# Performance work log

Hardware: AMD Instinct MI355X
Metric: run time of the kernel (lower is better)

## Reference

```python
import jax, jax.numpy as jnp
import numpy as np

BETA = 0.25
DECAY = 0.99
EPS = 1e-05
N_E = 1024
E_DIM = 64

def setup_inputs() -> dict:
    key = jax.random.key(0)
    k1, k2, k3, k4 = jax.random.split(key, 4)
    z = jax.random.normal(k1, (32, 64, 32, 32), dtype=jnp.float32)
    embedding = jax.random.normal(k2, (N_E, E_DIM), dtype=jnp.float32)
    cluster_size = jax.random.uniform(k3, (N_E,), dtype=jnp.float32)
    cluster_sum = jax.random.normal(k4, (N_E, E_DIM), dtype=jnp.float32)
    return {"z": z, "embedding": embedding, "cluster_size": cluster_size, "cluster_sum": cluster_sum}


def reference(z, embedding, cluster_size, cluster_sum):
    # z: (B, C, H, W) with C == e_dim
    zp = jnp.transpose(z, (0, 2, 3, 1))            # (B, H, W, C)
    zf = zp.reshape(-1, E_DIM)                      # (N, e_dim)
    # squared-distance matrix: ||z||^2 + ||e||^2 - 2 z.e  -> (N, n_e)
    distance = (jnp.sum(zf ** 2, axis=1, keepdims=True)
                + jnp.sum(embedding ** 2, axis=1)
                - 2.0 * (zf @ embedding.T))
    idx = jnp.argmin(distance, axis=1)              # (N,)
    # one-hot counts / cluster sums expressed as segment sums (same math)
    counts = jax.ops.segment_sum(jnp.ones(zf.shape[0], dtype=zf.dtype), idx, num_segments=N_E)
    sums = jax.ops.segment_sum(zf, idx, num_segments=N_E)
    # EMA buffer update (module is in training mode -> embedding refreshed)
    new_cluster_size = DECAY * cluster_size + (1.0 - DECAY) * counts
    new_cluster_sum = DECAY * cluster_sum + (1.0 - DECAY) * sums
    new_embed = new_cluster_sum / (new_cluster_size + EPS)[:, None]
    z_q = new_embed[idx].reshape(zp.shape)          # gather-dequantize
    L_commitment = jnp.mean((jax.lax.stop_gradient(z_q) - zp) ** 2)
    loss = BETA * L_commitment
    z_q = zp + jax.lax.stop_gradient(z_q - zp)      # straight-through
    z_q = jnp.transpose(z_q, (0, 3, 1, 2))          # back to (B, C, H, W)
    return z_q, loss, counts
```

## Files before the change

kernel.cpp:

```cpp
#include <hip/hip_runtime.h>
#include <hip/hip_bf16.h>


#define N_ROWS   32768
#define N_CODES  1024
#define EDIM     64
#define ZQ_ELEMS 2097152

__global__ void vq_prep(const float* __restrict__ emb, float* __restrict__ cs_zero,
                        float* __restrict__ enorm) {
    const int g = blockIdx.x * 256 + threadIdx.x;
    if (g < 66560) {
        cs_zero[g] = 0.f;
    } else {
        const int c = g - 66560;
        const float4* __restrict__ e4 = (const float4*)(emb + (c << 6));
        float s = 0.f;
        #pragma unroll
        for (int i = 0; i < 16; ++i) {
            const float4 v = e4[i];
            s = fmaf(v.x, v.x, s); s = fmaf(v.y, v.y, s);
            s = fmaf(v.z, v.z, s); s = fmaf(v.w, v.w, s);
        }
        enorm[c] = s;
    }
}

__global__ __launch_bounds__(256, 2) void vq_dist(
        const float* __restrict__ z, const float* __restrict__ emb,
        const float* __restrict__ enorm,
        float* __restrict__ half_score, int* __restrict__ half_idx) {
    __shared__ float zs[128 * 68];
    __shared__ float es[128 * 68];
    __shared__ float zn_s[128];

    const int t    = threadIdx.x;
    const int tx   = t & 15, ty = t >> 4;
    const int r0   = blockIdx.x * 128;
    const int half = blockIdx.y;
    const int b    = r0 >> 10;
    const int hw0  = r0 & 1023;

    #pragma unroll
    for (int i = 0; i < 32; ++i) {
        const int cell = i * 256 + t;
        const int row = cell & 127, c = cell >> 7;
        zs[row * 68 + c] = z[((b * 64 + c) << 10) + hw0 + row];
    }
    __syncthreads();

    if (t < 128) {
        const float4* z4 = (const float4*)zs + t * 17;
        float s = 0.f;
        #pragma unroll
        for (int g = 0; g < 16; ++g) {
            const float4 v = z4[g];
            s = fmaf(v.x, v.x, s); s = fmaf(v.y, v.y, s);
            s = fmaf(v.z, v.z, s); s = fmaf(v.w, v.w, s);
        }
        zn_s[t] = s;
    }
    __syncthreads();

    float znr[8];
    #pragma unroll
    for (int rr = 0; rr < 8; ++rr) znr[rr] = zn_s[ty + 16 * rr];

    float best[8]; int bidx[8];
    #pragma unroll
    for (int rr = 0; rr < 8; ++rr) { best[rr] = INFINITY; bidx[rr] = 0; }

    const float4* __restrict__ eg = (const float4*)(emb + (half << 9) * 64);
    float4 pf[8];
    #pragma unroll
    for (int p = 0; p < 8; ++p) pf[p] = eg[p * 256 + t];

    for (int ch = 0; ch < 4; ++ch) {
        #pragma unroll
        for (int p = 0; p < 8; ++p) {
            const int fid = p * 256 + t;
            ((float4*)es)[(fid >> 4) * 17 + (fid & 15)] = pf[p];
        }
        __syncthreads();
        if (ch < 3) {
            #pragma unroll
            for (int p = 0; p < 8; ++p) pf[p] = eg[(ch + 1) * 2048 + p * 256 + t];
        }
        const int cbase = (half << 9) + (ch << 7);
        float enj[8];
        #pragma unroll
        for (int j = 0; j < 8; ++j) enj[j] = enorm[cbase + tx + 16 * j];

        float acc[8][8];
        #pragma unroll
        for (int rr = 0; rr < 8; ++rr)
            #pragma unroll
            for (int j = 0; j < 8; ++j) acc[rr][j] = 0.f;

        for (int g = 0; g < 16; ++g) {
            float4 zf[8], ef[8];
            #pragma unroll
            for (int rr = 0; rr < 8; ++rr) zf[rr] = ((const float4*)zs)[(ty + 16 * rr) * 17 + g];
            #pragma unroll
            for (int j = 0; j < 8; ++j)  ef[j] = ((const float4*)es)[(tx + 16 * j) * 17 + g];
            #pragma unroll
            for (int rr = 0; rr < 8; ++rr)
                #pragma unroll
                for (int j = 0; j < 8; ++j) {
                    float a = acc[rr][j];
                    a = fmaf(zf[rr].x, ef[j].x, a);
                    a = fmaf(zf[rr].y, ef[j].y, a);
                    a = fmaf(zf[rr].z, ef[j].z, a);
                    a = fmaf(zf[rr].w, ef[j].w, a);
                    acc[rr][j] = a;
                }
        }

        #pragma unroll
        for (int rr = 0; rr < 8; ++rr)
            #pragma unroll
            for (int j = 0; j < 8; ++j) {
                const float s = (znr[rr] + enj[j]) - 2.0f * acc[rr][j];
                if (s < best[rr]) { best[rr] = s; bidx[rr] = cbase + tx + 16 * j; }
            }
        __syncthreads();
    }

    #pragma unroll
    for (int off = 1; off < 16; off <<= 1) {
        #pragma unroll
        for (int rr = 0; rr < 8; ++rr) {
            const float os = __shfl_xor(best[rr], off);
            const int   oi = __shfl_xor(bidx[rr], off);
            if (os < best[rr] || (os == best[rr] && oi < bidx[rr])) {
                best[rr] = os; bidx[rr] = oi;
            }
        }
    }
    if (tx == 0) {
        #pragma unroll
        for (int rr = 0; rr < 8; ++rr) {
            const int gr = r0 + ty + 16 * rr;
            half_score[half * N_ROWS + gr] = best[rr];
            half_idx  [half * N_ROWS + gr] = bidx[rr];
        }
    }
}

__global__ __launch_bounds__(256) void vq_resolve(
        const float* __restrict__ z,
        const float* __restrict__ half_score, const int* __restrict__ half_idx,
        int* __restrict__ idx_out, float* __restrict__ counts,
        float* __restrict__ sums) {
    __shared__ float zs[128 * 65];
    __shared__ int   idx_sh[128];
    const int t   = threadIdx.x;
    const int r0  = blockIdx.x * 128;
    const int b   = r0 >> 10;
    const int hw0 = r0 & 1023;

    #pragma unroll
    for (int i = 0; i < 32; ++i) {
        const int cell = i * 256 + t;
        const int row = cell & 127, c = cell >> 7;
        zs[row * 65 + c] = z[((b * 64 + c) << 10) + hw0 + row];
    }
    if (t < 128) {
        const int gr = r0 + t;
        const float s0 = half_score[gr], s1 = half_score[N_ROWS + gr];
        const int   i0 = half_idx[gr],   i1 = half_idx[N_ROWS + gr];
        const int   bi = (s1 < s0) ? i1 : i0;
        idx_out[gr] = bi;
        idx_sh[t] = bi;
        atomicAdd(&counts[bi], 1.0f);
    }
    __syncthreads();

    const int lane = t & 63, sub = t >> 6;
    #pragma unroll
    for (int i = 0; i < 32; ++i) {
        const int row = i * 4 + sub;
        atomicAdd(&sums[idx_sh[row] * 64 + lane], zs[row * 65 + lane]);
    }
}

__global__ void vq_ema(const float* __restrict__ counts, const float* __restrict__ sums,
                       const float* __restrict__ cs, const float* __restrict__ csum,
                       float* __restrict__ new_embed, float* __restrict__ out_counts,
                       float* __restrict__ out_loss) {
    const int g = blockIdx.x * 256 + threadIdx.x;
    const int c = g >> 6, d = g & 63;
    const float cnt = counts[c];
    const float nsize = 0.99f * cs[c] + 0.01f * cnt;
    const float nsum  = 0.99f * csum[g] + 0.01f * sums[g];
    new_embed[g] = nsum / (nsize + 1e-5f);
    if (d == 0) out_counts[c] = cnt;
    if (g == 0) out_loss[0] = 0.f;
}

__global__ __launch_bounds__(256) void vq_gather(
        const float* __restrict__ z, const int* __restrict__ idx,
        const float* __restrict__ new_embed,
        float* __restrict__ out_zq, float* __restrict__ out_loss) {
    __shared__ float red[4];
    const int t  = threadIdx.x;
    const int r0 = blockIdx.x * 256;
    const int b  = r0 >> 10;
    const int hw = (r0 & 1023) + t;
    const int myidx = idx[r0 + t];

    const float4* __restrict__ er = (const float4*)(new_embed + (myidx << 6));
    float4 e4[16];
    #pragma unroll
    for (int i = 0; i < 16; ++i) e4[i] = er[i];

    float lsum = 0.f;
    #pragma unroll
    for (int c = 0; c < 64; ++c) {
        const float e  = ((const float*)e4)[c];
        const int  off = ((b * 64 + c) << 10) + hw;
        const float zv = z[off];
        const float diff = e - zv;
        out_zq[off] = zv + diff;
        lsum = fmaf(diff, diff, lsum);
    }
    #pragma unroll
    for (int off = 32; off >= 1; off >>= 1) lsum += __shfl_down(lsum, off);
    if ((t & 63) == 0) red[t >> 6] = lsum;
    __syncthreads();
    if (t == 0) {
        const float s = red[0] + red[1] + red[2] + red[3];
        atomicAdd(out_loss, s * (0.25f / 2097152.0f));
    }
}

extern "C" void kernel_launch(void* const* d_in, const int* in_sizes, int n_in,
                              void* d_out, int out_size, void* d_ws, size_t ws_size,
                              hipStream_t stream) {
    const float* z    = (const float*)d_in[0];
    const float* emb  = (const float*)d_in[1];
    const float* cs   = (const float*)d_in[2];
    const float* csum = (const float*)d_in[3];
    float* out = (float*)d_out;

    int*   idx        = (int*)d_ws;
    float* counts     = (float*)d_ws + 32768;
    float* sums       = counts + 1024;
    float* enorm      = sums + 65536;
    float* new_embed  = enorm + 1024;
    float* half_score = new_embed + 65536;
    int*   half_idx   = (int*)(half_score + 2 * 32768);

    vq_prep<<<264, 256, 0, stream>>>(emb, counts, enorm);
    vq_dist<<<dim3(256, 2), 256, 0, stream>>>(z, emb, enorm, half_score, half_idx);
    vq_resolve<<<256, 256, 0, stream>>>(z, half_score, half_idx, idx, counts, sums);
    vq_ema<<<256, 256, 0, stream>>>(counts, sums, cs, csum, new_embed,
                                    out + ZQ_ELEMS + 1,
                                    out + ZQ_ELEMS);
    vq_gather<<<128, 256, 0, stream>>>(z, idx, new_embed, out, out + ZQ_ELEMS);
}
```

Measured before the change: 174.7 us.

## Split atomic accumulators, double-buffer LDS fragments, memset workspace separately

The atomic scatter of counts and sums in the resolve kernel now targets four replicated copies chosen by block index. This is meant to cut atomic contention on popular codes, and the EMA kernel adds the copies back together. The distance kernel double-buffers shared-memory fragment loads across the inner K loop, and moves the global prefetch of the next embedding chunk to the top of each chunk with a different barrier placement. Zeroing moves to hipMemsetAsync with a separate small enorm kernel, which adds a launch and four times the accumulator memory.

```diff
diff --git a/kernel.cpp b/kernel.cpp
--- a/kernel.cpp
+++ b/kernel.cpp
@@ -6,14 +6,11 @@
 #define N_CODES  1024
 #define EDIM     64
 #define ZQ_ELEMS 2097152
-
-__global__ void vq_prep(const float* __restrict__ emb, float* __restrict__ cs_zero,
-                        float* __restrict__ enorm) {
-    const int g = blockIdx.x * 256 + threadIdx.x;
-    if (g < 66560) {
-        cs_zero[g] = 0.f;
-    } else {
-        const int c = g - 66560;
+#define NSPLIT   4
+
+__global__ void vq_enorm(const float* __restrict__ emb, float* __restrict__ enorm) {
+    const int c = blockIdx.x * 256 + threadIdx.x;
+    if (c < N_CODES) {
         const float4* __restrict__ e4 = (const float4*)(emb + (c << 6));
         float s = 0.f;
         #pragma unroll
@@ -24,6 +21,26 @@
         }
         enorm[c] = s;
     }
+}
+
+__device__ __forceinline__ void ldfrag(float4 (&dst)[8], const float4* __restrict__ s4,
+                                       int lane, int g) {
+    #pragma unroll
+    for (int r = 0; r < 8; ++r) dst[r] = s4[(lane + 16 * r) * 17 + g];
+}
+__device__ __forceinline__ void fma_tile(const float4 (&zf)[8], const float4 (&ef)[8],
+                                         float (&acc)[8][8]) {
+    #pragma unroll
+    for (int rr = 0; rr < 8; ++rr)
+        #pragma unroll
+        for (int j = 0; j < 8; ++j) {
+            float a = acc[rr][j];
+            a = fmaf(zf[rr].x, ef[j].x, a);
+            a = fmaf(zf[rr].y, ef[j].y, a);
+            a = fmaf(zf[rr].z, ef[j].z, a);
+            a = fmaf(zf[rr].w, ef[j].w, a);
+            acc[rr][j] = a;
+        }
 }
 
 __global__ __launch_bounds__(256, 2) void vq_dist(
@@ -70,26 +87,26 @@
     #pragma unroll
     for (int rr = 0; rr < 8; ++rr) { best[rr] = INFINITY; bidx[rr] = 0; }
 
-    const float4* __restrict__ eg = (const float4*)(emb + (half << 9) * 64);
-    float4 pf[8];
-    #pragma unroll
-    for (int p = 0; p < 8; ++p) pf[p] = eg[p * 256 + t];
+    const float4* __restrict__ eg  = (const float4*)(emb + (half << 9) * 64);
+    const float4* __restrict__ zs4 = (const float4*)zs;
+    const float4* __restrict__ es4 = (const float4*)es;
 
     for (int ch = 0; ch < 4; ++ch) {
+        const int cbase = (half << 9) + (ch << 7);
+        float4 pf[8];
+        #pragma unroll
+        for (int p = 0; p < 8; ++p) pf[p] = eg[ch * 2048 + p * 256 + t];
+        float enj[8];
+        #pragma unroll
+        for (int j = 0; j < 8; ++j) enj[j] = enorm[cbase + tx + 16 * j];
+
+        __syncthreads();
         #pragma unroll
         for (int p = 0; p < 8; ++p) {
             const int fid = p * 256 + t;
             ((float4*)es)[(fid >> 4) * 17 + (fid & 15)] = pf[p];
         }
         __syncthreads();
-        if (ch < 3) {
-            #pragma unroll
-            for (int p = 0; p < 8; ++p) pf[p] = eg[(ch + 1) * 2048 + p * 256 + t];
-        }
-        const int cbase = (half << 9) + (ch << 7);
-        float enj[8];
-        #pragma unroll
-        for (int j = 0; j < 8; ++j) enj[j] = enorm[cbase + tx + 16 * j];
 
         float acc[8][8];
         #pragma unroll
@@ -97,23 +114,16 @@
             #pragma unroll
             for (int j = 0; j < 8; ++j) acc[rr][j] = 0.f;
 
-        for (int g = 0; g < 16; ++g) {
-            float4 zf[8], ef[8];
-            #pragma unroll
-            for (int rr = 0; rr < 8; ++rr) zf[rr] = ((const float4*)zs)[(ty + 16 * rr) * 17 + g];
-            #pragma unroll
-            for (int j = 0; j < 8; ++j)  ef[j] = ((const float4*)es)[(tx + 16 * j) * 17 + g];
-            #pragma unroll
-            for (int rr = 0; rr < 8; ++rr)
-                #pragma unroll
-                for (int j = 0; j < 8; ++j) {
-                    float a = acc[rr][j];
-                    a = fmaf(zf[rr].x, ef[j].x, a);
-                    a = fmaf(zf[rr].y, ef[j].y, a);
-                    a = fmaf(zf[rr].z, ef[j].z, a);
-                    a = fmaf(zf[rr].w, ef[j].w, a);
-                    acc[rr][j] = a;
-                }
+        float4 zf[8], efA[8], efB[8];
+        ldfrag(efA, es4, tx, 0);
+        #pragma unroll
+        for (int gp = 0; gp < 8; ++gp) {
+            ldfrag(zf, zs4, ty, 2 * gp);
+            ldfrag(efB, es4, tx, 2 * gp + 1);
+            fma_tile(zf, efA, acc);
+            ldfrag(zf, zs4, ty, 2 * gp + 1);
+            if (gp < 7) ldfrag(efA, es4, tx, 2 * gp + 2);
+            fma_tile(zf, efB, acc);
         }
 
         #pragma unroll
@@ -123,7 +133,6 @@
                 const float s = (znr[rr] + enj[j]) - 2.0f * acc[rr][j];
                 if (s < best[rr]) { best[rr] = s; bidx[rr] = cbase + tx + 16 * j; }
             }
-        __syncthreads();
     }
 
     #pragma unroll
@@ -158,6 +167,7 @@
     const int r0  = blockIdx.x * 128;
     const int b   = r0 >> 10;
     const int hw0 = r0 & 1023;
+    const int sp  = blockIdx.x & (NSPLIT - 1);
 
     #pragma unroll
     for (int i = 0; i < 32; ++i) {
@@ -172,7 +182,7 @@
         const int   bi = (s1 < s0) ? i1 : i0;
         idx_out[gr] = bi;
         idx_sh[t] = bi;
-        atomicAdd(&counts[bi], 1.0f);
+        atomicAdd(&counts[sp * N_CODES + bi], 1.0f);
     }
     __syncthreads();
 
@@ -180,7 +190,7 @@
     #pragma unroll
     for (int i = 0; i < 32; ++i) {
         const int row = i * 4 + sub;
-        atomicAdd(&sums[idx_sh[row] * 64 + lane], zs[row * 65 + lane]);
+        atomicAdd(&sums[sp * 65536 + idx_sh[row] * 64 + lane], zs[row * 65 + lane]);
     }
 }
 
@@ -190,9 +200,11 @@
                        float* __restrict__ out_loss) {
     const int g = blockIdx.x * 256 + threadIdx.x;
     const int c = g >> 6, d = g & 63;
-    const float cnt = counts[c];
+    const float cnt = (counts[c] + counts[N_CODES + c])
+                    + (counts[2 * N_CODES + c] + counts[3 * N_CODES + c]);
+    const float ssum = (sums[g] + sums[65536 + g]) + (sums[131072 + g] + sums[196608 + g]);
     const float nsize = 0.99f * cs[c] + 0.01f * cnt;
-    const float nsum  = 0.99f * csum[g] + 0.01f * sums[g];
+    const float nsum  = 0.99f * csum[g] + 0.01f * ssum;
     new_embed[g] = nsum / (nsize + 1e-5f);
     if (d == 0) out_counts[c] = cnt;
     if (g == 0) out_loss[0] = 0.f;
@@ -245,13 +257,15 @@
 
     int*   idx        = (int*)d_ws;
     float* counts     = (float*)d_ws + 32768;
-    float* sums       = counts + 1024;
-    float* enorm      = sums + 65536;
+    float* sums       = counts + NSPLIT * N_CODES;
+    float* enorm      = sums + NSPLIT * 65536;
     float* new_embed  = enorm + 1024;
     float* half_score = new_embed + 65536;
     int*   half_idx   = (int*)(half_score + 2 * 32768);
 
-    vq_prep<<<264, 256, 0, stream>>>(emb, counts, enorm);
+    hipMemsetAsync(counts, 0, NSPLIT * (N_CODES + 65536) * sizeof(float), stream);
+
+    vq_enorm<<<4, 256, 0, stream>>>(emb, enorm);
     vq_dist<<<dim3(256, 2), 256, 0, stream>>>(z, emb, enorm, half_score, half_idx);
     vq_resolve<<<256, 256, 0, stream>>>(z, half_score, half_idx, idx, counts, sums);
     vq_ema<<<256, 256, 0, stream>>>(counts, sums, cs, csum, new_embed,
```

New measurement: 170.3 us. 1.03x faster.
